# Kernel tuning notes

Measured on AMD Instinct MI355X. Metric: run time of the kernel, lower is better.

The kernel has to match this reference:

```python
import jax, jax.numpy as jnp
import numpy as np

EPS = 1e-6

def setup_inputs() -> dict:
    key = jax.random.key(0)
    k = jax.random.split(key, 7)
    N, E, d_i, d_o = 50000, 800000, 128, 128
    x = jax.random.normal(k[0], (N, d_i), dtype=jnp.float32)
    src = jax.random.randint(k[1], (E,), 0, N)
    tgt = jax.random.randint(k[2], (E,), 0, N)
    # xavier_uniform for both linear weights (torch nn.init.xavier_uniform_)
    lim_f = float(np.sqrt(6.0 / (2 * d_i + d_o)))
    Wf = jax.random.uniform(k[3], (d_o, 2 * d_i), jnp.float32, -lim_f, lim_f)
    lim_w = float(np.sqrt(6.0 / (2 * d_i + 1)))
    Ww = jax.random.uniform(k[4], (1, 2 * d_i), jnp.float32, -lim_w, lim_w)
    # torch Linear default bias init: U(-1/sqrt(fan_in), 1/sqrt(fan_in))
    lb = float(1.0 / np.sqrt(2 * d_i))
    bf = jax.random.uniform(k[5], (d_o,), jnp.float32, -lb, lb)
    bw = jax.random.uniform(k[6], (1,), jnp.float32, -lb, lb)
    return {"x": x, "Wf": Wf, "bf": bf, "Ww": Ww, "bw": bw,
            "src": src, "tgt": tgt, "num_nodes": N}


def reference(x, Wf, bf, Ww, bw, src, tgt, num_nodes):
    # gather endpoints and build edge features [E, 2*d_i]
    h = jnp.concatenate([x[src], x[tgt]], axis=1)
    # fused linear + relu message: [E, d_o]
    y = jax.nn.relu(h @ Wf.T + bf)
    # unnormalized attention score per edge: [E, 1]
    a = h @ Ww.T + bw
    # scatter-sum over target nodes (equivalent to mm(Mtgt, .))
    a_sum = jax.ops.segment_sum(a, tgt, num_segments=num_nodes) + EPS
    o = jax.ops.segment_sum(y * a, tgt, num_segments=num_nodes) / a_sum
    return o
```

## Files before the change

### kernel.cpp

```cpp
#include <hip/hip_runtime.h>


typedef short bf16x8 __attribute__((ext_vector_type(8)));
typedef short bf16x4 __attribute__((ext_vector_type(4)));
typedef float f32x4  __attribute__((ext_vector_type(4)));

__device__ inline short f32_to_bf16_rne(float f) {
    unsigned u = __float_as_uint(f);
    unsigned r = u + 0x7fffu + ((u >> 16) & 1u);
    return (short)(r >> 16);
}
__device__ inline float bf16s_to_f32(short s) {
    return __uint_as_float(((unsigned)(unsigned short)s) << 16);
}

__global__ __launch_bounds__(256) void k_wconv(
    const float* __restrict__ Wf, short* __restrict__ whp, short* __restrict__ wlp)
{
    int tid = blockIdx.x * 256 + threadIdx.x;
    if (tid >= 4096) return;
    int ct = tid >> 8, kt = (tid >> 6) & 3, lane = tid & 63;
    int c = ct * 16 + (lane & 15);
    int kbase = kt * 32 + (lane >> 4) * 8;
    bf16x8 h, l;
    #pragma unroll
    for (int j = 0; j < 8; ++j) {
        int k = kbase + j;
        float v = (c < 128) ? Wf[c * 256 + k] : Wf[(c - 128) * 256 + 128 + k];
        short hs = f32_to_bf16_rne(v);
        h[j] = hs;
        l[j] = f32_to_bf16_rne(v - bf16s_to_f32(hs));
    }
    *(bf16x8*)(whp + (size_t)tid * 8) = h;
    *(bf16x8*)(wlp + (size_t)tid * 8) = l;
}

__global__ __launch_bounds__(256) void k_pq(
    const float* __restrict__ x, const float* __restrict__ Ww,
    const float* __restrict__ bw, double* __restrict__ p,
    double* __restrict__ q, int N)
{
    int wid  = (blockIdx.x * 256 + threadIdx.x) >> 6;
    int lane = threadIdx.x & 63;
    if (wid >= N) return;
    const float* xr = x + (size_t)wid * 128;
    float x0 = xr[lane], x1 = xr[64 + lane];
    double ps = (double)x0 * (double)Ww[lane]       + (double)x1 * (double)Ww[64 + lane];
    double qs = (double)x0 * (double)Ww[128 + lane] + (double)x1 * (double)Ww[192 + lane];
    #pragma unroll
    for (int off = 32; off > 0; off >>= 1) {
        ps += __shfl_down(ps, off);
        qs += __shfl_down(qs, off);
    }
    if (lane == 0) { p[wid] = ps; q[wid] = qs + (double)bw[0]; }
}

__global__ __launch_bounds__(256) void k_transform(
    const float* __restrict__ x, const short* __restrict__ whp,
    const short* __restrict__ wlp, const float* __restrict__ bf,
    float* __restrict__ U, float* __restrict__ Vb, int N)
{
    __shared__ __attribute__((aligned(16))) char smem[32768];
    const int t = threadIdx.x, wv = t >> 6, lane = t & 63;
    const int n0 = blockIdx.x * 64;

    #pragma unroll
    for (int r = 0; r < 8; ++r) {
        int idx = r * 1024 + t * 4;
        int row = idx >> 7, col = idx & 127;
        int n = n0 + row;
        const float* sp = x + (size_t)((n < N) ? n : (N - 1)) * 128 + col;
        f32x4 v = *(const f32x4*)sp;
        bf16x4 hh, ll;
        #pragma unroll
        for (int j = 0; j < 4; ++j) {
            short hs = f32_to_bf16_rne(v[j]);
            hh[j] = hs;
            ll[j] = f32_to_bf16_rne(v[j] - bf16s_to_f32(hs));
        }
        int ba = (row * 256 + col * 2) ^ ((row & 7) << 4);
        *(bf16x4*)(smem + ba)         = hh;
        *(bf16x4*)(smem + 16384 + ba) = ll;
    }
    __syncthreads();

    f32x4 acc[4][4] = {};
    #pragma unroll
    for (int tt = 0; tt < 4; ++tt) {
        const int ct = wv * 4 + tt;
        bf16x8 Wh[4], Wl[4];
        #pragma unroll
        for (int kt = 0; kt < 4; ++kt) {
            size_t off = (size_t)((ct * 4 + kt) * 64 + lane) * 8;
            Wh[kt] = *(const bf16x8*)(whp + off);
            Wl[kt] = *(const bf16x8*)(wlp + off);
        }
        #pragma unroll
        for (int kt = 0; kt < 4; ++kt) {
            #pragma unroll
            for (int ns = 0; ns < 4; ++ns) {
                int row = ns * 16 + (lane & 15);
                int ba = (row * 256 + kt * 64 + (lane >> 4) * 16) ^ ((row & 7) << 4);
                bf16x8 xhf = *(const bf16x8*)(smem + ba);
                bf16x8 xlf = *(const bf16x8*)(smem + 16384 + ba);
                acc[tt][ns] = __builtin_amdgcn_mfma_f32_16x16x32_bf16(Wh[kt], xhf, acc[tt][ns], 0, 0, 0);
                acc[tt][ns] = __builtin_amdgcn_mfma_f32_16x16x32_bf16(Wh[kt], xlf, acc[tt][ns], 0, 0, 0);
                acc[tt][ns] = __builtin_amdgcn_mfma_f32_16x16x32_bf16(Wl[kt], xhf, acc[tt][ns], 0, 0, 0);
            }
        }
    }
    __syncthreads();

    if (wv < 2) {
        #pragma unroll
        for (int tt = 0; tt < 4; ++tt) {
            int cb = (wv * 4 + tt) * 64 + (lane >> 4) * 16;
            #pragma unroll
            for (int ns = 0; ns < 4; ++ns) {
                int node = ns * 16 + (lane & 15);
                int ba = (node * 512 + cb) ^ ((node & 7) << 4);
                *(f32x4*)(smem + ba) = acc[tt][ns];
            }
        }
    }
    __syncthreads();
    #pragma unroll
    for (int r = 0; r < 8; ++r) {
        int fo = r * 4096 + t * 16;
        int row = fo >> 9;
        if (n0 + row < N)
            *(f32x4*)(U + (size_t)(n0 + row) * 128 + ((fo & 511) >> 2)) =
                *(const f32x4*)(smem + (fo ^ ((row & 7) << 4)));
    }
    __syncthreads();

    if (wv >= 2) {
        #pragma unroll
        for (int tt = 0; tt < 4; ++tt) {
            int cb = ((wv - 2) * 4 + tt) * 64 + (lane >> 4) * 16;
            #pragma unroll
            for (int ns = 0; ns < 4; ++ns) {
                int node = ns * 16 + (lane & 15);
                int ba = (node * 512 + cb) ^ ((node & 7) << 4);
                *(f32x4*)(smem + ba) = acc[tt][ns];
            }
        }
    }
    __syncthreads();
    #pragma unroll
    for (int r = 0; r < 8; ++r) {
        int fo = r * 4096 + t * 16;
        int row = fo >> 9;
        int col = (fo & 511) >> 2;
        if (n0 + row < N) {
            f32x4 v = *(const f32x4*)(smem + (fo ^ ((row & 7) << 4)));
            f32x4 bias = *(const f32x4*)(bf + col);
            v[0] += bias[0]; v[1] += bias[1]; v[2] += bias[2]; v[3] += bias[3];
            *(f32x4*)(Vb + (size_t)(n0 + row) * 128 + col) = v;
        }
    }
}


__global__ __launch_bounds__(256) void k_hist(
    const int* __restrict__ tgt, int* __restrict__ counts, int E)
{
    int e = blockIdx.x * 256 + threadIdx.x;
    if (e < E) atomicAdd(&counts[tgt[e]], 1);
}

__global__ __launch_bounds__(256) void k_scan1(
    const int* __restrict__ counts, int* __restrict__ incl,
    int* __restrict__ partials, int N)
{
    __shared__ int sh[256];
    int t = threadIdx.x;
    int i = blockIdx.x * 256 + t;
    int v = (i < N) ? counts[i] : 0;
    sh[t] = v;
    __syncthreads();
    #pragma unroll
    for (int off = 1; off < 256; off <<= 1) {
        int add = (t >= off) ? sh[t - off] : 0;
        __syncthreads();
        sh[t] += add;
        __syncthreads();
    }
    if (i < N) incl[i] = sh[t];
    if (t == 255) partials[blockIdx.x] = sh[255];
}

__global__ __launch_bounds__(256) void k_scan2(int* __restrict__ partials, int nb)
{
    __shared__ int sh[256];
    int t = threadIdx.x;
    int v = (t < nb) ? partials[t] : 0;
    sh[t] = v;
    __syncthreads();
    #pragma unroll
    for (int off = 1; off < 256; off <<= 1) {
        int add = (t >= off) ? sh[t - off] : 0;
        __syncthreads();
        sh[t] += add;
        __syncthreads();
    }
    if (t < nb) partials[t] = sh[t] - v;
}

__global__ __launch_bounds__(256) void k_scan3(
    const int* __restrict__ counts, const int* __restrict__ incl,
    const int* __restrict__ partials, int* __restrict__ offsets,
    int* __restrict__ cursor, int N)
{
    int i = blockIdx.x * 256 + threadIdx.x;
    if (i >= N) return;
    int off = incl[i] - counts[i] + partials[i >> 8];
    offsets[i] = off;
    cursor[i]  = off;
}

__global__ __launch_bounds__(256) void k_scatter(
    const int* __restrict__ src, const int* __restrict__ tgt,
    int* __restrict__ cursor, int* __restrict__ srcs, int E)
{
    int e = blockIdx.x * 256 + threadIdx.x;
    if (e >= E) return;
    int pos = atomicAdd(&cursor[tgt[e]], 1);
    srcs[pos] = src[e];
}


__global__ __launch_bounds__(256) void k_node(
    const float* __restrict__ U, const float* __restrict__ Vb,
    const double* __restrict__ p, const double* __restrict__ q,
    const int* __restrict__ offsets, const int* __restrict__ counts,
    const int* __restrict__ srcs, float* __restrict__ out, int N)
{
    int idx  = blockIdx.x * 256 + threadIdx.x;
    int n    = idx >> 5;
    int lane = threadIdx.x & 31;
    if (n >= N) return;

    float4 Vn = ((const float4*)(Vb + (size_t)n * 128))[lane];
    double qn = q[n];
    int beg = offsets[n];
    int cnt = counts[n];

    double ax = 0.0, ay = 0.0, az = 0.0, aw = 0.0, asum = 0.0;

    int i = 0;
    for (; i + 4 <= cnt; i += 4) {
        int s0 = srcs[beg + i + 0];
        int s1 = srcs[beg + i + 1];
        int s2 = srcs[beg + i + 2];
        int s3 = srcs[beg + i + 3];
        float4 U0 = ((const float4*)(U + (size_t)s0 * 128))[lane];
        float4 U1 = ((const float4*)(U + (size_t)s1 * 128))[lane];
        float4 U2 = ((const float4*)(U + (size_t)s2 * 128))[lane];
        float4 U3 = ((const float4*)(U + (size_t)s3 * 128))[lane];
        double a0 = p[s0] + qn, a1 = p[s1] + qn, a2 = p[s2] + qn, a3 = p[s3] + qn;
        float f0 = (float)a0, f1 = (float)a1, f2 = (float)a2, f3 = (float)a3;

        ax += (double)(fmaxf(U0.x + Vn.x, 0.f) * f0);
        ay += (double)(fmaxf(U0.y + Vn.y, 0.f) * f0);
        az += (double)(fmaxf(U0.z + Vn.z, 0.f) * f0);
        aw += (double)(fmaxf(U0.w + Vn.w, 0.f) * f0);
        asum += a0;
        ax += (double)(fmaxf(U1.x + Vn.x, 0.f) * f1);
        ay += (double)(fmaxf(U1.y + Vn.y, 0.f) * f1);
        az += (double)(fmaxf(U1.z + Vn.z, 0.f) * f1);
        aw += (double)(fmaxf(U1.w + Vn.w, 0.f) * f1);
        asum += a1;
        ax += (double)(fmaxf(U2.x + Vn.x, 0.f) * f2);
        ay += (double)(fmaxf(U2.y + Vn.y, 0.f) * f2);
        az += (double)(fmaxf(U2.z + Vn.z, 0.f) * f2);
        aw += (double)(fmaxf(U2.w + Vn.w, 0.f) * f2);
        asum += a2;
        ax += (double)(fmaxf(U3.x + Vn.x, 0.f) * f3);
        ay += (double)(fmaxf(U3.y + Vn.y, 0.f) * f3);
        az += (double)(fmaxf(U3.z + Vn.z, 0.f) * f3);
        aw += (double)(fmaxf(U3.w + Vn.w, 0.f) * f3);
        asum += a3;
    }
    for (; i < cnt; ++i) {
        int s = srcs[beg + i];
        float4 Ue = ((const float4*)(U + (size_t)s * 128))[lane];
        double a = p[s] + qn;
        float af = (float)a;
        ax += (double)(fmaxf(Ue.x + Vn.x, 0.f) * af);
        ay += (double)(fmaxf(Ue.y + Vn.y, 0.f) * af);
        az += (double)(fmaxf(Ue.z + Vn.z, 0.f) * af);
        aw += (double)(fmaxf(Ue.w + Vn.w, 0.f) * af);
        asum += a;
    }

    double inv = 1.0 / (asum + 1e-6);
    float4 o;
    o.x = (float)(ax * inv);
    o.y = (float)(ay * inv);
    o.z = (float)(az * inv);
    o.w = (float)(aw * inv);
    ((float4*)(out + (size_t)n * 128))[lane] = o;
}

extern "C" void kernel_launch(void* const* d_in, const int* in_sizes, int n_in,
                              void* d_out, int out_size, void* d_ws, size_t ws_size,
                              hipStream_t stream)
{
    const float* x   = (const float*)d_in[0];
    const float* Wf  = (const float*)d_in[1];
    const float* bf  = (const float*)d_in[2];
    const float* Ww  = (const float*)d_in[3];
    const float* bw  = (const float*)d_in[4];
    const int*   src = (const int*)d_in[5];
    const int*   tgt = (const int*)d_in[6];

    const int N = in_sizes[0] / 128;
    const int E = in_sizes[5];
    float* out = (float*)d_out;

    char* w = (char*)d_ws;
    float*  U        = (float*)w;                 w += (size_t)N * 128 * sizeof(float);
    float*  Vb       = (float*)w;                 w += (size_t)N * 128 * sizeof(float);
    double* p        = (double*)w;                w += (size_t)N * sizeof(double);
    double* q        = (double*)w;                w += (size_t)N * sizeof(double);
    int*    counts   = (int*)w;                   w += (size_t)N * sizeof(int);
    int*    incl     = (int*)w;                   w += (size_t)N * sizeof(int);
    int*    offsets  = (int*)w;                   w += (size_t)N * sizeof(int);
    int*    cursor   = (int*)w;                   w += (size_t)N * sizeof(int);
    int*    partials = (int*)w;                   w += 4096;
    int*    srcs     = (int*)w;                   w += (size_t)E * sizeof(int);
    short*  whp      = (short*)w;                 w += 256 * 128 * sizeof(short);
    short*  wlp      = (short*)w;

    hipMemsetAsync(counts, 0, (size_t)N * sizeof(int), stream);

    k_wconv<<<16, 256, 0, stream>>>(Wf, whp, wlp);
    k_pq<<<(N * 64 + 255) / 256, 256, 0, stream>>>(x, Ww, bw, p, q, N);
    k_transform<<<(N + 63) / 64, 256, 0, stream>>>(x, whp, wlp, bf, U, Vb, N);

    int ebk = (E + 255) / 256;
    int nbk = (N + 255) / 256;
    k_hist<<<ebk, 256, 0, stream>>>(tgt, counts, E);
    k_scan1<<<nbk, 256, 0, stream>>>(counts, incl, partials, N);
    k_scan2<<<1, 256, 0, stream>>>(partials, nbk);
    k_scan3<<<nbk, 256, 0, stream>>>(counts, incl, partials, offsets, cursor, N);
    k_scatter<<<ebk, 256, 0, stream>>>(src, tgt, cursor, srcs, E);

    long long nthreads = (long long)N * 32;
    k_node<<<(int)((nthreads + 255) / 256), 256, 0, stream>>>(
        U, Vb, p, q, offsets, counts, srcs, out, N);
}
```

Baseline: 272.5 us.

## Store U in bf16, accumulate in fp32, fuse p/q dot into transform

```diff
diff --git a/kernel.cpp b/kernel.cpp
--- a/kernel.cpp
+++ b/kernel.cpp
@@ -35,30 +35,12 @@
     *(bf16x8*)(wlp + (size_t)tid * 8) = l;
 }
 
-__global__ __launch_bounds__(256) void k_pq(
-    const float* __restrict__ x, const float* __restrict__ Ww,
-    const float* __restrict__ bw, double* __restrict__ p,
-    double* __restrict__ q, int N)
-{
-    int wid  = (blockIdx.x * 256 + threadIdx.x) >> 6;
-    int lane = threadIdx.x & 63;
-    if (wid >= N) return;
-    const float* xr = x + (size_t)wid * 128;
-    float x0 = xr[lane], x1 = xr[64 + lane];
-    double ps = (double)x0 * (double)Ww[lane]       + (double)x1 * (double)Ww[64 + lane];
-    double qs = (double)x0 * (double)Ww[128 + lane] + (double)x1 * (double)Ww[192 + lane];
-    #pragma unroll
-    for (int off = 32; off > 0; off >>= 1) {
-        ps += __shfl_down(ps, off);
-        qs += __shfl_down(qs, off);
-    }
-    if (lane == 0) { p[wid] = ps; q[wid] = qs + (double)bw[0]; }
-}
-
 __global__ __launch_bounds__(256) void k_transform(
     const float* __restrict__ x, const short* __restrict__ whp,
     const short* __restrict__ wlp, const float* __restrict__ bf,
-    float* __restrict__ U, float* __restrict__ Vb, int N)
+    const float* __restrict__ Ww, const float* __restrict__ bw,
+    short* __restrict__ Ub, float* __restrict__ Vb,
+    double* __restrict__ p, double* __restrict__ q, int N)
 {
     __shared__ __attribute__((aligned(16))) char smem[32768];
     const int t = threadIdx.x, wv = t >> 6, lane = t & 63;
@@ -81,6 +63,29 @@
         int ba = (row * 256 + col * 2) ^ ((row & 7) << 4);
         *(bf16x4*)(smem + ba)         = hh;
         *(bf16x4*)(smem + 16384 + ba) = ll;
+    }
+
+    {
+        int row = wv * 16 + (lane >> 2);
+        int n = n0 + row;
+        int c0 = (lane & 3) * 32;
+        const float* xr = x + (size_t)((n < N) ? n : (N - 1)) * 128 + c0;
+        double ps = 0.0, qs = 0.0;
+        #pragma unroll
+        for (int jj = 0; jj < 32; jj += 4) {
+            f32x4 v = *(const f32x4*)(xr + jj);
+            #pragma unroll
+            for (int j = 0; j < 4; ++j) {
+                ps += (double)v[j] * (double)Ww[c0 + jj + j];
+                qs += (double)v[j] * (double)Ww[128 + c0 + jj + j];
+            }
+        }
+        ps += __shfl_xor(ps, 1); ps += __shfl_xor(ps, 2);
+        qs += __shfl_xor(qs, 1); qs += __shfl_xor(qs, 2);
+        if ((lane & 3) == 0 && n < N) {
+            p[n] = ps;
+            q[n] = qs + (double)bw[0];
+        }
     }
     __syncthreads();
 
@@ -128,9 +133,14 @@
     for (int r = 0; r < 8; ++r) {
         int fo = r * 4096 + t * 16;
         int row = fo >> 9;
-        if (n0 + row < N)
-            *(f32x4*)(U + (size_t)(n0 + row) * 128 + ((fo & 511) >> 2)) =
-                *(const f32x4*)(smem + (fo ^ ((row & 7) << 4)));
+        int col = (fo & 511) >> 2;
+        if (n0 + row < N) {
+            f32x4 v = *(const f32x4*)(smem + (fo ^ ((row & 7) << 4)));
+            bf16x4 b;
+            b[0] = f32_to_bf16_rne(v[0]); b[1] = f32_to_bf16_rne(v[1]);
+            b[2] = f32_to_bf16_rne(v[2]); b[3] = f32_to_bf16_rne(v[3]);
+            *(bf16x4*)(Ub + (size_t)(n0 + row) * 128 + col) = b;
+        }
     }
     __syncthreads();
 
@@ -231,7 +241,7 @@
 
 
 __global__ __launch_bounds__(256) void k_node(
-    const float* __restrict__ U, const float* __restrict__ Vb,
+    const short* __restrict__ Ub, const float* __restrict__ Vb,
     const double* __restrict__ p, const double* __restrict__ q,
     const int* __restrict__ offsets, const int* __restrict__ counts,
     const int* __restrict__ srcs, float* __restrict__ out, int N)
@@ -246,7 +256,8 @@
     int beg = offsets[n];
     int cnt = counts[n];
 
-    double ax = 0.0, ay = 0.0, az = 0.0, aw = 0.0, asum = 0.0;
+    float ax = 0.f, ay = 0.f, az = 0.f, aw = 0.f;
+    double asum = 0.0;
 
     int i = 0;
     for (; i + 4 <= cnt; i += 4) {
@@ -254,52 +265,52 @@
         int s1 = srcs[beg + i + 1];
         int s2 = srcs[beg + i + 2];
         int s3 = srcs[beg + i + 3];
-        float4 U0 = ((const float4*)(U + (size_t)s0 * 128))[lane];
-        float4 U1 = ((const float4*)(U + (size_t)s1 * 128))[lane];
-        float4 U2 = ((const float4*)(U + (size_t)s2 * 128))[lane];
-        float4 U3 = ((const float4*)(U + (size_t)s3 * 128))[lane];
+        bf16x4 u0 = *(const bf16x4*)(Ub + (size_t)s0 * 128 + lane * 4);
+        bf16x4 u1 = *(const bf16x4*)(Ub + (size_t)s1 * 128 + lane * 4);
+        bf16x4 u2 = *(const bf16x4*)(Ub + (size_t)s2 * 128 + lane * 4);
+        bf16x4 u3 = *(const bf16x4*)(Ub + (size_t)s3 * 128 + lane * 4);
         double a0 = p[s0] + qn, a1 = p[s1] + qn, a2 = p[s2] + qn, a3 = p[s3] + qn;
         float f0 = (float)a0, f1 = (float)a1, f2 = (float)a2, f3 = (float)a3;
 
-        ax += (double)(fmaxf(U0.x + Vn.x, 0.f) * f0);
-        ay += (double)(fmaxf(U0.y + Vn.y, 0.f) * f0);
-        az += (double)(fmaxf(U0.z + Vn.z, 0.f) * f0);
-        aw += (double)(fmaxf(U0.w + Vn.w, 0.f) * f0);
+        ax += fmaxf(bf16s_to_f32(u0[0]) + Vn.x, 0.f) * f0;
+        ay += fmaxf(bf16s_to_f32(u0[1]) + Vn.y, 0.f) * f0;
+        az += fmaxf(bf16s_to_f32(u0[2]) + Vn.z, 0.f) * f0;
+        aw += fmaxf(bf16s_to_f32(u0[3]) + Vn.w, 0.f) * f0;
         asum += a0;
-        ax += (double)(fmaxf(U1.x + Vn.x, 0.f) * f1);
-        ay += (double)(fmaxf(U1.y + Vn.y, 0.f) * f1);
-        az += (double)(fmaxf(U1.z + Vn.z, 0.f) * f1);
-        aw += (double)(fmaxf(U1.w + Vn.w, 0.f) * f1);
+        ax += fmaxf(bf16s_to_f32(u1[0]) + Vn.x, 0.f) * f1;
+        ay += fmaxf(bf16s_to_f32(u1[1]) + Vn.y, 0.f) * f1;
+        az += fmaxf(bf16s_to_f32(u1[2]) + Vn.z, 0.f) * f1;
+        aw += fmaxf(bf16s_to_f32(u1[3]) + Vn.w, 0.f) * f1;
         asum += a1;
-        ax += (double)(fmaxf(U2.x + Vn.x, 0.f) * f2);
-        ay += (double)(fmaxf(U2.y + Vn.y, 0.f) * f2);
-        az += (double)(fmaxf(U2.z + Vn.z, 0.f) * f2);
-        aw += (double)(fmaxf(U2.w + Vn.w, 0.f) * f2);
+        ax += fmaxf(bf16s_to_f32(u2[0]) + Vn.x, 0.f) * f2;
+        ay += fmaxf(bf16s_to_f32(u2[1]) + Vn.y, 0.f) * f2;
+        az += fmaxf(bf16s_to_f32(u2[2]) + Vn.z, 0.f) * f2;
+        aw += fmaxf(bf16s_to_f32(u2[3]) + Vn.w, 0.f) * f2;
         asum += a2;
-        ax += (double)(fmaxf(U3.x + Vn.x, 0.f) * f3);
-        ay += (double)(fmaxf(U3.y + Vn.y, 0.f) * f3);
-        az += (double)(fmaxf(U3.z + Vn.z, 0.f) * f3);
-        aw += (double)(fmaxf(U3.w + Vn.w, 0.f) * f3);
+        ax += fmaxf(bf16s_to_f32(u3[0]) + Vn.x, 0.f) * f3;
+        ay += fmaxf(bf16s_to_f32(u3[1]) + Vn.y, 0.f) * f3;
+        az += fmaxf(bf16s_to_f32(u3[2]) + Vn.z, 0.f) * f3;
+        aw += fmaxf(bf16s_to_f32(u3[3]) + Vn.w, 0.f) * f3;
         asum += a3;
     }
     for (; i < cnt; ++i) {
         int s = srcs[beg + i];
-        float4 Ue = ((const float4*)(U + (size_t)s * 128))[lane];
+        bf16x4 u = *(const bf16x4*)(Ub + (size_t)s * 128 + lane * 4);
         double a = p[s] + qn;
         float af = (float)a;
-        ax += (double)(fmaxf(Ue.x + Vn.x, 0.f) * af);
-        ay += (double)(fmaxf(Ue.y + Vn.y, 0.f) * af);
-        az += (double)(fmaxf(Ue.z + Vn.z, 0.f) * af);
-        aw += (double)(fmaxf(Ue.w + Vn.w, 0.f) * af);
+        ax += fmaxf(bf16s_to_f32(u[0]) + Vn.x, 0.f) * af;
+        ay += fmaxf(bf16s_to_f32(u[1]) + Vn.y, 0.f) * af;
+        az += fmaxf(bf16s_to_f32(u[2]) + Vn.z, 0.f) * af;
+        aw += fmaxf(bf16s_to_f32(u[3]) + Vn.w, 0.f) * af;
         asum += a;
     }
 
     double inv = 1.0 / (asum + 1e-6);
     float4 o;
-    o.x = (float)(ax * inv);
-    o.y = (float)(ay * inv);
-    o.z = (float)(az * inv);
-    o.w = (float)(aw * inv);
+    o.x = (float)((double)ax * inv);
+    o.y = (float)((double)ay * inv);
+    o.z = (float)((double)az * inv);
+    o.w = (float)((double)aw * inv);
     ((float4*)(out + (size_t)n * 128))[lane] = o;
 }
 
@@ -320,7 +331,7 @@
     float* out = (float*)d_out;
 
     char* w = (char*)d_ws;
-    float*  U        = (float*)w;                 w += (size_t)N * 128 * sizeof(float);
+    short*  Ub       = (short*)w;                 w += (size_t)N * 128 * sizeof(short);
     float*  Vb       = (float*)w;                 w += (size_t)N * 128 * sizeof(float);
     double* p        = (double*)w;                w += (size_t)N * sizeof(double);
     double* q        = (double*)w;                w += (size_t)N * sizeof(double);
@@ -336,8 +347,8 @@
     hipMemsetAsync(counts, 0, (size_t)N * sizeof(int), stream);
 
     k_wconv<<<16, 256, 0, stream>>>(Wf, whp, wlp);
-    k_pq<<<(N * 64 + 255) / 256, 256, 0, stream>>>(x, Ww, bw, p, q, N);
-    k_transform<<<(N + 63) / 64, 256, 0, stream>>>(x, whp, wlp, bf, U, Vb, N);
+    k_transform<<<(N + 63) / 64, 256, 0, stream>>>(
+        x, whp, wlp, bf, Ww, bw, Ub, Vb, p, q, N);
 
     int ebk = (E + 255) / 256;
     int nbk = (N + 255) / 256;
@@ -349,5 +360,5 @@
 
     long long nthreads = (long long)N * 32;
     k_node<<<(int)((nthreads + 255) / 256), 256, 0, stream>>>(
-        U, Vb, p, q, offsets, counts, srcs, out, N);
-}
+        Ub, Vb, p, q, offsets, counts, srcs, out, N);
+}
```

Result: faster. 252.0 us (-7.5%).
